# Kernel tuning notes

Measured on AMD Instinct MI355X. Metric: run time of the kernel, lower is better.

## Reference

```python
import jax, jax.numpy as jnp
import numpy as np

N_NODES = 200000
N_EDGES = 800000
IN_CH = 128
OUT_CH = 64
MAX_DEG = 4
N_GRAPHS = 8192


def setup_inputs() -> dict:
    key = jax.random.key(0)
    k1, k2, k3, k4, k5 = jax.random.split(key, 5)
    x = jax.random.normal(k1, (N_NODES, IN_CH), dtype=jnp.float32)
    edge_index = jax.random.randint(k2, (2, N_EDGES), 0, N_NODES, dtype=jnp.int64)
    batch = jnp.sort(jax.random.randint(k3, (N_NODES,), 0, N_GRAPHS, dtype=jnp.int64))
    # MFConv: one neighbor-lin and one root-lin per degree bucket (0..max_degree)
    W_lin = jax.random.normal(k4, (MAX_DEG + 1, IN_CH, OUT_CH), dtype=jnp.float32) / np.sqrt(IN_CH)
    W_root = jax.random.normal(k5, (MAX_DEG + 1, IN_CH, OUT_CH), dtype=jnp.float32) / np.sqrt(IN_CH)
    return {"x": x, "edge_index": edge_index, "batch": batch, "W_lin": W_lin, "W_root": W_root}


def reference(x, edge_index, batch, W_lin, W_root):
    src, dst = edge_index[0], edge_index[1]
    n = x.shape[0]
    # sum-aggregate neighbor features at target nodes (MFConv aggr='add')
    agg = jax.ops.segment_sum(x[src], dst, num_segments=n)  # [N, in]
    # node in-degree, clamped to max_degree
    deg = jax.ops.segment_sum(jnp.ones_like(dst, dtype=jnp.int32), dst, num_segments=n)
    deg = jnp.minimum(deg, MAX_DEG)  # [N]
    # degree-bucketed per-node linear transforms
    out = jnp.zeros((n, W_lin.shape[-1]), dtype=x.dtype)
    for d in range(MAX_DEG + 1):
        mask = (deg == d)[:, None]
        out = out + jnp.where(mask, agg @ W_lin[d] + x @ W_root[d], 0.0)
    out = jax.nn.relu(out)
    out = jax.nn.softmax(out, axis=1)
    # global add pool over graphs
    pooled = jax.ops.segment_sum(out, batch, num_segments=N_GRAPHS)  # [G, out]
    return pooled
```

## Files before the change

kernel.cpp:

```cpp
#include <hip/hip_runtime.h>
#include <hip/hip_bf16.h>

#define NN 200000
#define NE 800000
#define ICH 128
#define OCH 64
#define MAXD 4
#define NG 8192

#define SLOTS 24
#define NCLS 16
#define HIST_BLOCKS 196

#define XB_BLOCKS 25000
#define ED_BLOCKS 3125
#define PREP_BLOCKS (XB_BLOCKS + ED_BLOCKS + 5)

typedef __attribute__((ext_vector_type(8))) short bf16x8;
typedef __attribute__((ext_vector_type(4))) float f32x4;

static const size_t OFF_XB   = 0;
static const size_t OFF_WT   = 51200000;
static const size_t OFF_DEG  = 51363840;
static const size_t OFF_SLOT = 52163840;
static const size_t OFF_NL   = 71363840;
static const size_t OFF_CTR  = 72163840;

__device__ inline unsigned pack_bf16(float lo, float hi) {
    unsigned short a = __bfloat16_as_ushort(__float2bfloat16(lo));
    unsigned short b = __bfloat16_as_ushort(__float2bfloat16(hi));
    return ((unsigned)b << 16) | (unsigned)a;
}

__device__ inline float b2f(short s) {
    unsigned u = ((unsigned)(unsigned short)s) << 16;
    float f;
    __builtin_memcpy(&f, &u, 4);
    return f;
}

__global__ void k_prep(const float* __restrict__ x, const int* __restrict__ ei,
                       const float* __restrict__ Wl, const float* __restrict__ Wr,
                       uint2* __restrict__ xb, unsigned* __restrict__ wt,
                       int* __restrict__ deg, int* __restrict__ slot) {
    int b = blockIdx.x;
    int tid = threadIdx.x;
    if (b < XB_BLOCKS) {
        int i = b * 256 + tid;
        float4 v = ((const float4*)x)[i];
        xb[i] = make_uint2(pack_bf16(v.x, v.y), pack_bf16(v.z, v.w));
    } else if (b < XB_BLOCKS + ED_BLOCKS) {
        int e = (b - XB_BLOCKS) * 256 + tid;
        int src = ei[e];
        int dst = ei[NE + e];
        int pos = atomicAdd(&deg[dst], 1);
        if (pos < SLOTS) slot[dst * SLOTS + pos] = src;
    } else {
        int bk = b - XB_BLOCKS - ED_BLOCKS;
        int ch = tid & 63;
        int k0 = (tid >> 6) * 64;
        unsigned* dst = wt + ((size_t)bk * 64 + ch) * 128;
        for (int k = k0; k < k0 + 64; k += 2) {
            float f0 = (k < 128) ? Wl[(size_t)bk * 8192 + (size_t)k * 64 + ch]
                                 : Wr[(size_t)bk * 8192 + (size_t)(k - 128) * 64 + ch];
            float f1 = (k + 1 < 128) ? Wl[(size_t)bk * 8192 + (size_t)(k + 1) * 64 + ch]
                                     : Wr[(size_t)bk * 8192 + (size_t)(k + 1 - 128) * 64 + ch];
            dst[k >> 1] = pack_bf16(f0, f1);
        }
    }
}

__global__ void k_hist(const int* __restrict__ deg, int* __restrict__ bcnt16) {
    __shared__ int cnt[NCLS];
    int tid = threadIdx.x;
    if (tid < NCLS) cnt[tid] = 0;
    __syncthreads();
    int i0 = blockIdx.x * 1024 + tid * 4;
    #pragma unroll
    for (int j = 0; j < 4; ++j) {
        int i = i0 + j;
        if (i < NN) {
            int d = deg[i];
            atomicAdd(&cnt[d < 15 ? d : 15], 1);
        }
    }
    __syncthreads();
    if (tid < NCLS && cnt[tid]) atomicAdd(&bcnt16[tid], cnt[tid]);
}

__global__ void k_part(const int* __restrict__ deg, const int* __restrict__ bcnt16,
                       int* __restrict__ gfill16, int* __restrict__ nlist,
                       int* __restrict__ bcnt5) {
    __shared__ int cnt[NCLS];
    __shared__ int base[NCLS];
    __shared__ int coff[NCLS];
    int tid = threadIdx.x;
    if (tid < NCLS) cnt[tid] = 0;
    __syncthreads();
    int i0 = blockIdx.x * 1024 + tid * 4;
    int cls[4], lp[4];
    #pragma unroll
    for (int j = 0; j < 4; ++j) {
        int i = i0 + j;
        if (i < NN) {
            int d = deg[i];
            cls[j] = d < 15 ? d : 15;
            lp[j] = atomicAdd(&cnt[cls[j]], 1);
        }
    }
    __syncthreads();
    if (tid < NCLS) base[tid] = atomicAdd(&gfill16[tid], cnt[tid]);
    if (tid == 0) {
        const int order[NCLS] = {0, 1, 2, 3, 15, 14, 13, 12, 11, 10, 9, 8, 7, 6, 5, 4};
        int r = 0;
        #pragma unroll
        for (int q = 0; q < NCLS; ++q) { coff[order[q]] = r; r += bcnt16[order[q]]; }
        if (blockIdx.x == 0) {
            bcnt5[0] = bcnt16[0]; bcnt5[1] = bcnt16[1];
            bcnt5[2] = bcnt16[2]; bcnt5[3] = bcnt16[3];
            int s = 0;
            #pragma unroll
            for (int c = 4; c < 16; ++c) s += bcnt16[c];
            bcnt5[4] = s;
        }
    }
    __syncthreads();
    #pragma unroll
    for (int j = 0; j < 4; ++j) {
        int i = i0 + j;
        if (i < NN) nlist[coff[cls[j]] + base[cls[j]] + lp[j]] = i;
    }
}

__launch_bounds__(256, 2)
__global__ void k_gemm(const unsigned short* __restrict__ xb,
                       const int* __restrict__ slot,
                       const int* __restrict__ deg,
                       const unsigned short* __restrict__ wt,
                       const int* __restrict__ nlist, const int* __restrict__ bcnt,
                       const int* __restrict__ batch, float* __restrict__ out) {
    __shared__ int gid_s[64];
    __shared__ int nid_s[64];
    __shared__ int dc_s[64];

    int cnt[5];
    #pragma unroll
    for (int b = 0; b < 5; ++b) cnt[b] = bcnt[b];
    int bt = blockIdx.x;
    int bucket = -1, nstart = 0, count = 0;
    int t0 = 0, o = 0;
    #pragma unroll
    for (int b = 0; b < 5; ++b) {
        int tb = (cnt[b] + 63) >> 6;
        if (bucket < 0 && bt < t0 + tb) {
            bucket = b;
            int local = bt - t0;
            nstart = o + local * 64;
            count = cnt[b] - local * 64;
            if (count > 64) count = 64;
        }
        t0 += tb;
        o += cnt[b];
    }
    if (bucket < 0) return;

    int tid = threadIdx.x;
    int w = tid >> 6, lane = tid & 63;
    if (tid < 64) {
        int nd = (tid < count) ? nlist[nstart + tid] : -1;
        nid_s[tid] = nd;
        gid_s[tid] = (nd >= 0) ? batch[nd] : -1;
        int d = (nd >= 0) ? deg[nd] : 0;
        dc_s[tid] = d < SLOTS ? d : SLOTS;
    }
    __syncthreads();

    int arow = lane & 15;
    int kgrp = lane >> 4;
    int wnode = w * 16;
    int row = wnode + arow;

    int nd = nid_s[row];
    int dc = dc_s[row];
    const int* sl = slot + (size_t)(nd < 0 ? 0 : nd) * SLOTS;

    float fa[32];
    #pragma unroll
    for (int i = 0; i < 32; ++i) fa[i] = 0.f;
    for (int j = 0; j < dc; ++j) {
        int sn = sl[j];
        const bf16x8* rb = (const bf16x8*)(xb + (size_t)sn * 128);
        #pragma unroll
        for (int kk = 0; kk < 4; ++kk) {
            bf16x8 v = rb[kk * 4 + kgrp];
            #pragma unroll
            for (int e = 0; e < 8; ++e) fa[kk * 8 + e] += b2f(v[e]);
        }
    }

    bf16x8 afrag[8];
    #pragma unroll
    for (int kk = 0; kk < 4; ++kk) {
        bf16x8 t;
        #pragma unroll
        for (int e = 0; e < 8; ++e)
            t[e] = (short)__bfloat16_as_ushort(__float2bfloat16(fa[kk * 8 + e]));
        afrag[kk] = t;
    }
    if (nd >= 0) {
        const bf16x8* ro = (const bf16x8*)(xb + (size_t)nd * 128);
        #pragma unroll
        for (int kk = 0; kk < 4; ++kk) afrag[kk + 4] = ro[kk * 4 + kgrp];
    } else {
        bf16x8 z = {0, 0, 0, 0, 0, 0, 0, 0};
        #pragma unroll
        for (int kk = 0; kk < 4; ++kk) afrag[kk + 4] = z;
    }

    const unsigned short* wb = wt + (size_t)bucket * 16384;

    f32x4 acc[4];
    #pragma unroll
    for (int s = 0; s < 4; ++s) acc[s] = (f32x4){0.f, 0.f, 0.f, 0.f};

    #pragma unroll
    for (int kk = 0; kk < 8; ++kk) {
        int kw = kk * 32 + kgrp * 8;
        #pragma unroll
        for (int s = 0; s < 4; ++s) {
            int ch = s * 16 + arow;
            bf16x8 bv = *(const bf16x8*)(wb + (size_t)ch * 256 + kw);
            acc[s] = __builtin_amdgcn_mfma_f32_16x16x32_bf16(afrag[kk], bv, acc[s], 0, 0, 0);
        }
    }

    #pragma unroll
    for (int r = 0; r < 4; ++r) {
        float v0 = fmaxf(acc[0][r], 0.f);
        float v1 = fmaxf(acc[1][r], 0.f);
        float v2 = fmaxf(acc[2][r], 0.f);
        float v3 = fmaxf(acc[3][r], 0.f);
        float m = fmaxf(fmaxf(v0, v1), fmaxf(v2, v3));
        #pragma unroll
        for (int d = 1; d < 16; d <<= 1) m = fmaxf(m, __shfl_xor(m, d, 16));
        float e0 = __expf(v0 - m), e1 = __expf(v1 - m);
        float e2 = __expf(v2 - m), e3 = __expf(v3 - m);
        float ssum = e0 + e1 + e2 + e3;
        #pragma unroll
        for (int d = 1; d < 16; d <<= 1) ssum += __shfl_xor(ssum, d, 16);
        float inv = 1.0f / ssum;
        acc[0][r] = e0 * inv; acc[1][r] = e1 * inv;
        acc[2][r] = e2 * inv; acc[3][r] = e3 * inv;
    }

    int nl0 = wnode + kgrp * 4;
    int g0 = gid_s[nl0], g1 = gid_s[nl0 + 1], g2 = gid_s[nl0 + 2], g3 = gid_s[nl0 + 3];
    int ch0 = lane & 15;
    #pragma unroll
    for (int s = 0; s < 4; ++s) {
        float* ob = out + s * 16 + ch0;
        float run = acc[s][0];
        int gp = g0;
        if (g1 != gp) { if (gp >= 0) atomicAdd(ob + (size_t)gp * 64, run); run = 0.f; gp = g1; }
        run += acc[s][1];
        if (g2 != gp) { if (gp >= 0) atomicAdd(ob + (size_t)gp * 64, run); run = 0.f; gp = g2; }
        run += acc[s][2];
        if (g3 != gp) { if (gp >= 0) atomicAdd(ob + (size_t)gp * 64, run); run = 0.f; gp = g3; }
        run += acc[s][3];
        if (gp >= 0) atomicAdd(ob + (size_t)gp * 64, run);
    }
}

extern "C" void kernel_launch(void* const* d_in, const int* in_sizes, int n_in,
                              void* d_out, int out_size, void* d_ws, size_t ws_size,
                              hipStream_t stream) {
    const float* x = (const float*)d_in[0];
    const int* ei = (const int*)d_in[1];
    const int* batch = (const int*)d_in[2];
    const float* Wl = (const float*)d_in[3];
    const float* Wr = (const float*)d_in[4];
    float* out = (float*)d_out;
    char* ws = (char*)d_ws;

    unsigned* xb = (unsigned*)(ws + OFF_XB);
    unsigned* wt = (unsigned*)(ws + OFF_WT);
    int* deg = (int*)(ws + OFF_DEG);
    int* slot = (int*)(ws + OFF_SLOT);
    int* nlist = (int*)(ws + OFF_NL);
    int* ctr = (int*)(ws + OFF_CTR);
    int* bcnt16 = ctr + 0;
    int* gfill16 = ctr + 16;
    int* bcnt5 = ctr + 32;

    hipMemsetAsync(deg, 0, (size_t)NN * 4, stream);
    hipMemsetAsync(ctr, 0, 256, stream);
    hipMemsetAsync(out, 0, (size_t)NG * OCH * 4, stream);

    k_prep<<<PREP_BLOCKS, 256, 0, stream>>>(x, ei, Wl, Wr, (uint2*)xb, wt, deg, slot);
    k_hist<<<HIST_BLOCKS, 256, 0, stream>>>(deg, bcnt16);
    k_part<<<HIST_BLOCKS, 256, 0, stream>>>(deg, bcnt16, gfill16, nlist, bcnt5);
    k_gemm<<<3130, 256, 0, stream>>>((const unsigned short*)xb, slot, deg,
                                     (const unsigned short*)wt, nlist, bcnt5, batch, out);
}
```

Baseline: 325.9 us.

## Partition edge scatter by destination range and enlarge gemm blocks to 128 nodes

The edge-scatter phase now has each block scan a 2048-edge chunk and handle only edges whose destination lies in one of eight node ranges. Degree atomics and slot writes from concurrently running blocks therefore stay in a narrower address window, improving cache locality, but every chunk reads the dst index eight times. The scatter blocks are also placed before the x-to-bf16 conversion. Separately, the gemm kernel goes from 256 threads and 64 nodes per block to 512 threads and 128 nodes, halving the grid and the per-block setup, with launch bounds relaxed accordingly.

```diff
diff --git a/kernel.cpp b/kernel.cpp
--- a/kernel.cpp
+++ b/kernel.cpp
@@ -12,9 +12,11 @@
 #define NCLS 16
 #define HIST_BLOCKS 196
 
+#define ED_CHUNKS 391
+#define ED8_BLOCKS (ED_CHUNKS * 8)
 #define XB_BLOCKS 25000
-#define ED_BLOCKS 3125
-#define PREP_BLOCKS (XB_BLOCKS + ED_BLOCKS + 5)
+#define PREP_BLOCKS (ED8_BLOCKS + XB_BLOCKS + 5)
+#define DST_PER_GRP 25000
 
 typedef __attribute__((ext_vector_type(8))) short bf16x8;
 typedef __attribute__((ext_vector_type(4))) float f32x4;
@@ -45,18 +47,30 @@
                        int* __restrict__ deg, int* __restrict__ slot) {
     int b = blockIdx.x;
     int tid = threadIdx.x;
-    if (b < XB_BLOCKS) {
-        int i = b * 256 + tid;
+    if (b < ED8_BLOCKS) {
+        int grp = b & 7;
+        int chunk = b >> 3;
+        int lo = grp * DST_PER_GRP;
+        int hi = lo + DST_PER_GRP;
+        int e0 = chunk * 2048 + tid;
+        #pragma unroll
+        for (int it = 0; it < 8; ++it) {
+            int e = e0 + it * 256;
+            if (e < NE) {
+                int dst = ei[NE + e];
+                if (dst >= lo && dst < hi) {
+                    int src = ei[e];
+                    int pos = atomicAdd(&deg[dst], 1);
+                    if (pos < SLOTS) slot[dst * SLOTS + pos] = src;
+                }
+            }
+        }
+    } else if (b < ED8_BLOCKS + XB_BLOCKS) {
+        int i = (b - ED8_BLOCKS) * 256 + tid;
         float4 v = ((const float4*)x)[i];
         xb[i] = make_uint2(pack_bf16(v.x, v.y), pack_bf16(v.z, v.w));
-    } else if (b < XB_BLOCKS + ED_BLOCKS) {
-        int e = (b - XB_BLOCKS) * 256 + tid;
-        int src = ei[e];
-        int dst = ei[NE + e];
-        int pos = atomicAdd(&deg[dst], 1);
-        if (pos < SLOTS) slot[dst * SLOTS + pos] = src;
     } else {
-        int bk = b - XB_BLOCKS - ED_BLOCKS;
+        int bk = b - ED8_BLOCKS - XB_BLOCKS;
         int ch = tid & 63;
         int k0 = (tid >> 6) * 64;
         unsigned* dst = wt + ((size_t)bk * 64 + ch) * 128;
@@ -132,16 +146,16 @@
     }
 }
 
-__launch_bounds__(256, 2)
+__launch_bounds__(512)
 __global__ void k_gemm(const unsigned short* __restrict__ xb,
                        const int* __restrict__ slot,
                        const int* __restrict__ deg,
                        const unsigned short* __restrict__ wt,
                        const int* __restrict__ nlist, const int* __restrict__ bcnt,
                        const int* __restrict__ batch, float* __restrict__ out) {
-    __shared__ int gid_s[64];
-    __shared__ int nid_s[64];
-    __shared__ int dc_s[64];
+    __shared__ int gid_s[128];
+    __shared__ int nid_s[128];
+    __shared__ int dc_s[128];
 
     int cnt[5];
     #pragma unroll
@@ -151,13 +165,13 @@
     int t0 = 0, o = 0;
     #pragma unroll
     for (int b = 0; b < 5; ++b) {
-        int tb = (cnt[b] + 63) >> 6;
+        int tb = (cnt[b] + 127) >> 7;
         if (bucket < 0 && bt < t0 + tb) {
             bucket = b;
             int local = bt - t0;
-            nstart = o + local * 64;
-            count = cnt[b] - local * 64;
-            if (count > 64) count = 64;
+            nstart = o + local * 128;
+            count = cnt[b] - local * 128;
+            if (count > 128) count = 128;
         }
         t0 += tb;
         o += cnt[b];
@@ -166,7 +180,7 @@
 
     int tid = threadIdx.x;
     int w = tid >> 6, lane = tid & 63;
-    if (tid < 64) {
+    if (tid < 128) {
         int nd = (tid < count) ? nlist[nstart + tid] : -1;
         nid_s[tid] = nd;
         gid_s[tid] = (nd >= 0) ? batch[nd] : -1;
@@ -299,6 +313,6 @@
     k_prep<<<PREP_BLOCKS, 256, 0, stream>>>(x, ei, Wl, Wr, (uint2*)xb, wt, deg, slot);
     k_hist<<<HIST_BLOCKS, 256, 0, stream>>>(deg, bcnt16);
     k_part<<<HIST_BLOCKS, 256, 0, stream>>>(deg, bcnt16, gfill16, nlist, bcnt5);
-    k_gemm<<<3130, 256, 0, stream>>>((const unsigned short*)xb, slot, deg,
+    k_gemm<<<1567, 512, 0, stream>>>((const unsigned short*)xb, slot, deg,
                                      (const unsigned short*)wt, nlist, bcnt5, batch, out);
 }
```

After: 310.9 us. -4.6%, faster.
